# Optimization experiments

Hardware: AMD Instinct MI355X
Metric: run time of the kernel (lower is better)

## Reference

```python
import jax, jax.numpy as jnp
import numpy as np

H = 128          # hidden_size == in_channels == graph_hidden_size
P = 16           # pair_neurons
B = 4096         # number of graph pairs
T = 262144       # total nodes per side
V_D, V_P, V_A = 10000, 4000, 4000          # leaf vocab sizes
NG_D, NG_P, NG_A = 13000, 5200, 5200       # DAG graph node counts
L_D, L_P, L_A = 4, 4, 5                    # ancestor levels
TOTAL_V = V_D + V_P + V_A                  # 18000 rows in all_embedding


def setup_inputs() -> dict:
    key = jax.random.key(0)
    ks = jax.random.split(key, 40)
    n = lambda i, shape, s: jax.random.normal(ks[i], shape, jnp.float32) * s
    ri = lambda i, shape, hi: jax.random.randint(ks[i], shape, 0, hi, dtype=jnp.int64)
    inp = {}
    # forward args
    inp["left_x"] = ri(0, (T, 1), TOTAL_V)
    inp["left_graph_index"] = ri(1, (B,), B)
    inp["right_x"] = ri(2, (T, 1), TOTAL_V)
    inp["right_graph_index"] = ri(3, (B,), B)
    inp["left_x_batch"] = jnp.sort(ri(4, (T,), B))
    inp["right_x_batch"] = jnp.sort(ri(5, (T,), B))
    inp["left_diag_cnt"] = ri(6, (B,), 64)
    inp["right_diag_cnt"] = ri(7, (B,), 64)
    # DAG structure buffers (built by build_ancestors in the original)
    inp["anc_d"] = ri(8, (V_D, L_D), NG_D)
    inp["leaf_d"] = ri(9, (V_D, L_D), NG_D)
    inp["anc_p"] = ri(10, (V_P, L_P), NG_P)
    inp["leaf_p"] = ri(11, (V_P, L_P), NG_P)
    inp["anc_a"] = ri(12, (V_A, L_A), NG_A)
    inp["leaf_a"] = ri(13, (V_A, L_A), NG_A)
    # learned parameters
    inp["emb_d"] = n(14, (NG_D, H), 0.1)
    inp["emb_p"] = n(15, (NG_P, H), 0.1)
    inp["emb_a"] = n(16, (NG_A, H), 0.1)
    inp["Wl_d"] = n(17, (H, 2 * H), 0.05); inp["bl_d"] = n(18, (H,), 0.05); inp["ap_d"] = n(19, (H, 1), 0.05)
    inp["Wl_p"] = n(20, (H, 2 * H), 0.05); inp["bl_p"] = n(21, (H,), 0.05); inp["ap_p"] = n(22, (H, 1), 0.05)
    inp["Wl_a"] = n(23, (H, 2 * H), 0.05); inp["bl_a"] = n(24, (H,), 0.05); inp["ap_a"] = n(25, (H, 1), 0.05)
    inp["W_ntn"] = n(26, (H, H, P), 0.02)
    inp["V_ntn"] = n(27, (P, 2 * H), 0.02)
    inp["b_ntn"] = n(28, (P,), 0.02)
    inp["w_fc"] = n(29, (1, P), 0.1)
    inp["b_fc"] = n(30, (1,), 0.1)
    return inp


def _dag_embedding(emb, anc, leaf, Wl, bl, ap):
    # emb: [Ng,H]; anc/leaf: [V,L] int
    anc_e = emb[anc]    # [V,L,H]
    leaf_e = emb[leaf]  # [V,L,H]
    h = jnp.tanh(jnp.concatenate([anc_e, leaf_e], axis=-1) @ Wl.T + bl)  # [V,L,H]
    aw = (h @ ap)[..., 0]                     # [V,L]
    s = jax.nn.softmax(aw, axis=-1)           # [V,L]
    # torch.matmul((V,L),(V,L,C)).sum(dim=1) == einsum('l,vlc->vc', s.sum(0), anc_e)
    return jnp.einsum('l,vlc->vc', s.sum(axis=0), anc_e)  # [V,H]


def reference(left_x, left_graph_index, right_x, right_graph_index,
              left_x_batch, right_x_batch, left_diag_cnt, right_diag_cnt,
              anc_d, leaf_d, anc_p, leaf_p, anc_a, leaf_a,
              emb_d, emb_p, emb_a,
              Wl_d, bl_d, ap_d, Wl_p, bl_p, ap_p, Wl_a, bl_a, ap_a,
              W_ntn, V_ntn, b_ntn, w_fc, b_fc):
    all_emb = jnp.concatenate([
        _dag_embedding(emb_d, anc_d, leaf_d, Wl_d, bl_d, ap_d),
        _dag_embedding(emb_p, anc_p, leaf_p, Wl_p, bl_p, ap_p),
        _dag_embedding(emb_a, anc_a, leaf_a, Wl_a, bl_a, ap_a),
    ], axis=0)                                  # [TOTAL_V, H]
    left_onto = all_emb[left_x[:, 0]]           # [T,H]
    right_onto = all_emb[right_x[:, 0]]         # [T,H]
    le = jax.ops.segment_sum(left_onto, left_x_batch, num_segments=B)    # [B,H]
    re = jax.ops.segment_sum(right_onto, right_x_batch, num_segments=B)  # [B,H]
    # Neural tensor similarity: tanh(e1^T W_k e2 + V [e1;e2] + b)
    bilinear = jnp.einsum('bi,ijp,bj->bp', le, W_ntn, re)                # [B,P]
    block = jnp.concatenate([le, re], axis=-1) @ V_ntn.T                 # [B,P]
    pair_sim = jnp.tanh(bilinear + block + b_ntn)                        # [B,P]
    out = jax.nn.sigmoid(pair_sim @ w_fc.T + b_fc)[:, 0]                 # [B]
    return out
```

## Files before the change

kernel.cpp:

```cpp
#include <hip/hip_runtime.h>
#include <hip/hip_bf16.h>

typedef __hip_bfloat16 bf16;
typedef __attribute__((ext_vector_type(8))) short bf16x8;
typedef __attribute__((ext_vector_type(4))) float f32x4;

#define HID 128
#define PD  16
#define BB  4096
#define TT  262144
#define VD  10000
#define VP  4000
#define VA  4000
#define NGD 13000
#define NGP 5200
#define NGA 5200

#define NB_D ((NGD + 31) / 32)
#define NB_P ((NGP + 31) / 32)
#define NB_A ((NGA + 31) / 32)

__device__ __forceinline__ float2 bf2x(unsigned int u) {
    float lo = __uint_as_float(u << 16);
    float hi = __uint_as_float(u & 0xffff0000u);
    return make_float2(lo, hi);
}

union Pack2 { bf16 h[2]; unsigned int u; };
__device__ __forceinline__ unsigned int pk2(float a, float b) {
    Pack2 p; p.h[0] = __float2bfloat16(a); p.h[1] = __float2bfloat16(b); return p.u;
}

__global__ __launch_bounds__(256) void prep_b3(
    const float* __restrict__ Wl_d, const float* __restrict__ Wl_p, const float* __restrict__ Wl_a,
    bf16* __restrict__ B3_d, bf16* __restrict__ B3_p, bf16* __restrict__ B3_a)
{
    const int sec = blockIdx.x >> 4, jt = blockIdx.x & 15;
    const float* Wl = (sec == 0) ? Wl_d : (sec == 1) ? Wl_p : Wl_a;
    bf16* B3 = (sec == 0) ? B3_d : (sec == 1) ? B3_p : B3_a;
    const int tid = threadIdx.x;
    const int q = tid >> 6, lane = tid & 63;
    const int quad = lane >> 4, m = lane & 15;
    const int col = jt * 16 + m;
    const float* src = (col < 128) ? (Wl + col * 256) : (Wl + (col - 128) * 256 + 128);
    unsigned int pk[4];
#pragma unroll
    for (int jp = 0; jp < 4; ++jp) {
        int k0 = q * 32 + quad * 8 + 2 * jp;
        pk[jp] = pk2(src[k0], src[k0 + 1]);
    }
    uint4 val = make_uint4(pk[0], pk[1], pk[2], pk[3]);
    *reinterpret_cast<uint4*>(B3 + ((size_t)(jt * 4 + q) * 64 + lane) * 8) = val;
}

__device__ __forceinline__ void stage1_body(
    unsigned short (*Abf)[136],
    const float* __restrict__ emb, const bf16* __restrict__ B3,
    bf16* __restrict__ U, int NG, int blk)
{
    const int tid  = threadIdx.x;
    const int row0 = blk * 32;
    {
        const int r = tid >> 3, seg = tid & 7;
        const int g = row0 + r;
        float v[16];
        if (g < NG) {
            const float4* src = reinterpret_cast<const float4*>(emb + (size_t)g * HID + seg * 16);
#pragma unroll
            for (int i = 0; i < 4; ++i) {
                float4 f = src[i];
                v[4 * i] = f.x; v[4 * i + 1] = f.y; v[4 * i + 2] = f.z; v[4 * i + 3] = f.w;
            }
        } else {
#pragma unroll
            for (int i = 0; i < 16; ++i) v[i] = 0.f;
        }
        unsigned int pk[8];
#pragma unroll
        for (int i = 0; i < 8; ++i) pk[i] = pk2(v[2 * i], v[2 * i + 1]);
        uint4* dst = reinterpret_cast<uint4*>(&Abf[r][seg * 16]);
        dst[0] = make_uint4(pk[0], pk[1], pk[2], pk[3]);
        dst[1] = make_uint4(pk[4], pk[5], pk[6], pk[7]);
    }
    __syncthreads();

    const int lane   = tid & 63;
    const int w      = tid >> 6;
    const int gtile  = w & 1;
    const int jstrip = w >> 1;
    const int lrow   = gtile * 16 + (lane & 15);
    const int koff   = (lane >> 4) * 8;
    const bf16x8* B3f = reinterpret_cast<const bf16x8*>(B3);

    f32x4 acc[8];
#pragma unroll
    for (int t = 0; t < 8; ++t) acc[t] = (f32x4){0.f, 0.f, 0.f, 0.f};

#pragma unroll
    for (int q = 0; q < 4; ++q) {
        bf16x8 ef = *reinterpret_cast<const bf16x8*>(&Abf[lrow][q * 32 + koff]);
#pragma unroll
        for (int t = 0; t < 8; ++t) {
            int jt = jstrip * 8 + t;
            bf16x8 wf = B3f[(jt * 4 + q) * 64 + lane];
            acc[t] = __builtin_amdgcn_mfma_f32_16x16x32_bf16(wf, ef, acc[t], 0, 0, 0);
        }
    }

    const int g = row0 + gtile * 16 + (lane & 15);
    if (g < NG) {
        const int quad = lane >> 4;
        bf16* Ur = U + (size_t)g * 256;
#pragma unroll
        for (int t = 0; t < 8; ++t) {
            int j0 = (jstrip * 8 + t) * 16 + quad * 4;
            uint2 st = make_uint2(pk2(acc[t].x, acc[t].y), pk2(acc[t].z, acc[t].w));
            *reinterpret_cast<uint2*>(Ur + j0) = st;
        }
    }
}

__global__ __launch_bounds__(256) void stage1_mfma(
    const float* __restrict__ emb_d, const bf16* __restrict__ B3_d, bf16* __restrict__ U_d,
    const float* __restrict__ emb_p, const bf16* __restrict__ B3_p, bf16* __restrict__ U_p,
    const float* __restrict__ emb_a, const bf16* __restrict__ B3_a, bf16* __restrict__ U_a)
{
    __shared__ unsigned short Abf[32][136];
    int bx = blockIdx.x;
    if (bx < NB_D)             stage1_body(Abf, emb_d, B3_d, U_d, NGD, bx);
    else if (bx < NB_D + NB_P) stage1_body(Abf, emb_p, B3_p, U_p, NGP, bx - NB_D);
    else                       stage1_body(Abf, emb_a, B3_a, U_a, NGA, bx - NB_D - NB_P);
}

template <int L>
__device__ __forceinline__ void aw_body(
    float* sacc,
    const bf16* __restrict__ U, const int* __restrict__ anc, const int* __restrict__ leaf,
    const float* __restrict__ bl, const float* __restrict__ ap,
    float* __restrict__ s_out, int V, int blk, int nblk)
{
    const int tid  = threadIdx.x;
    const int lane = tid & 63;
    const int wid  = blk * 4 + (tid >> 6);
    const int nw   = nblk * 4;
    const float2 blv = *reinterpret_cast<const float2*>(bl + 2 * lane);
    const float2 apv = *reinterpret_cast<const float2*>(ap + 2 * lane);
    const unsigned int* Uw = reinterpret_cast<const unsigned int*>(U);
    float wacc[L];
#pragma unroll
    for (int l = 0; l < L; ++l) wacc[l] = 0.f;

    for (int vp = wid; vp < V / 2; vp += nw) {
        const int v0 = 2 * vp;
        int a0[L], f0[L], a1[L], f1[L];
        if (L == 4) {
            int4 ia = *reinterpret_cast<const int4*>(anc  + (size_t)v0 * 4);
            int4 ib = *reinterpret_cast<const int4*>(anc  + (size_t)v0 * 4 + 4);
            int4 fa = *reinterpret_cast<const int4*>(leaf + (size_t)v0 * 4);
            int4 fb = *reinterpret_cast<const int4*>(leaf + (size_t)v0 * 4 + 4);
            a0[0] = ia.x; a0[1] = ia.y; a0[2] = ia.z; a0[3] = ia.w;
            a1[0] = ib.x; a1[1] = ib.y; a1[2] = ib.z; a1[3] = ib.w;
            f0[0] = fa.x; f0[1] = fa.y; f0[2] = fa.z; f0[3] = fa.w;
            f1[0] = fb.x; f1[1] = fb.y; f1[2] = fb.z; f1[3] = fb.w;
        } else {
#pragma unroll
            for (int l = 0; l < L; ++l) {
                a0[l] = anc[(size_t)v0 * L + l];
                a1[l] = anc[(size_t)(v0 + 1) * L + l];
                f0[l] = leaf[(size_t)v0 * L + l];
                f1[l] = leaf[(size_t)(v0 + 1) * L + l];
            }
        }
        unsigned int ua0[L], ul0[L], ua1[L], ul1[L];
#pragma unroll
        for (int l = 0; l < L; ++l) {
            ua0[l] = Uw[(size_t)a0[l] * 128 + lane];
            ul0[l] = Uw[(size_t)f0[l] * 128 + 64 + lane];
            ua1[l] = Uw[(size_t)a1[l] * 128 + lane];
            ul1[l] = Uw[(size_t)f1[l] * 128 + 64 + lane];
        }
        float aw0[L], aw1[L];
#pragma unroll
        for (int l = 0; l < L; ++l) {
            float2 x0 = bf2x(ua0[l]), y0 = bf2x(ul0[l]);
            float2 x1 = bf2x(ua1[l]), y1 = bf2x(ul1[l]);
            float p0 = tanhf(x0.x + y0.x + blv.x) * apv.x + tanhf(x0.y + y0.y + blv.y) * apv.y;
            float p1 = tanhf(x1.x + y1.x + blv.x) * apv.x + tanhf(x1.y + y1.y + blv.y) * apv.y;
#pragma unroll
            for (int off = 32; off; off >>= 1) {
                p0 += __shfl_xor(p0, off, 64);
                p1 += __shfl_xor(p1, off, 64);
            }
            aw0[l] = p0; aw1[l] = p1;
        }
        float m0 = aw0[0], m1 = aw1[0];
#pragma unroll
        for (int l = 1; l < L; ++l) { m0 = fmaxf(m0, aw0[l]); m1 = fmaxf(m1, aw1[l]); }
        float d0 = 0.f, d1 = 0.f, e0[L], e1[L];
#pragma unroll
        for (int l = 0; l < L; ++l) {
            e0[l] = __expf(aw0[l] - m0); d0 += e0[l];
            e1[l] = __expf(aw1[l] - m1); d1 += e1[l];
        }
        float i0 = 1.f / d0, i1 = 1.f / d1;
#pragma unroll
        for (int l = 0; l < L; ++l) wacc[l] += e0[l] * i0 + e1[l] * i1;
    }
    if (lane == 0) {
#pragma unroll
        for (int l = 0; l < L; ++l) atomicAdd(&sacc[l], wacc[l]);
    }
    __syncthreads();
    if (tid < L) atomicAdd(&s_out[tid], sacc[tid]);
}

__global__ __launch_bounds__(256) void aw_all(
    const bf16* __restrict__ U_d, const int* __restrict__ anc_d, const int* __restrict__ leaf_d,
    const float* __restrict__ bl_d, const float* __restrict__ ap_d,
    const bf16* __restrict__ U_p, const int* __restrict__ anc_p, const int* __restrict__ leaf_p,
    const float* __restrict__ bl_p, const float* __restrict__ ap_p,
    const bf16* __restrict__ U_a, const int* __restrict__ anc_a, const int* __restrict__ leaf_a,
    const float* __restrict__ bl_a, const float* __restrict__ ap_a,
    float* __restrict__ s_sum)
{
    __shared__ float sacc[5];
    const int tid = threadIdx.x;
    if (tid < 5) sacc[tid] = 0.f;
    __syncthreads();
    int bx = blockIdx.x;
    if (bx < 512)      aw_body<4>(sacc, U_d, anc_d, leaf_d, bl_d, ap_d, s_sum + 0, VD, bx, 512);
    else if (bx < 768) aw_body<4>(sacc, U_p, anc_p, leaf_p, bl_p, ap_p, s_sum + 4, VP, bx - 512, 256);
    else               aw_body<5>(sacc, U_a, anc_a, leaf_a, bl_a, ap_a, s_sum + 8, VA, bx - 768, 256);
}

template <int L>
__device__ __forceinline__ void allemb_body(
    const float* __restrict__ emb, const int* __restrict__ anc,
    const float* __restrict__ s, float* __restrict__ out, int V, int blk, int nblk)
{
    const int tid   = threadIdx.x;
    const int lane4 = tid & 31;
    const int vslot = tid >> 5;
    const float4* emb4 = reinterpret_cast<const float4*>(emb);
    float4* out4 = reinterpret_cast<float4*>(out);
    float sv[L];
#pragma unroll
    for (int l = 0; l < L; ++l) sv[l] = s[l];
    for (int vp = blk * 8 + vslot; vp < V / 2; vp += nblk * 8) {
        const int v0 = 2 * vp;
        int a0[L], a1[L];
        if (L == 4) {
            int4 ia = *reinterpret_cast<const int4*>(anc + (size_t)v0 * 4);
            int4 ib = *reinterpret_cast<const int4*>(anc + (size_t)v0 * 4 + 4);
            a0[0] = ia.x; a0[1] = ia.y; a0[2] = ia.z; a0[3] = ia.w;
            a1[0] = ib.x; a1[1] = ib.y; a1[2] = ib.z; a1[3] = ib.w;
        } else {
#pragma unroll
            for (int l = 0; l < L; ++l) {
                a0[l] = anc[(size_t)v0 * L + l];
                a1[l] = anc[(size_t)(v0 + 1) * L + l];
            }
        }
        float4 e0[L], e1[L];
#pragma unroll
        for (int l = 0; l < L; ++l) {
            e0[l] = emb4[(size_t)a0[l] * 32 + lane4];
            e1[l] = emb4[(size_t)a1[l] * 32 + lane4];
        }
        float4 r0 = make_float4(0.f, 0.f, 0.f, 0.f);
        float4 r1 = make_float4(0.f, 0.f, 0.f, 0.f);
#pragma unroll
        for (int l = 0; l < L; ++l) {
            r0.x += sv[l] * e0[l].x; r0.y += sv[l] * e0[l].y;
            r0.z += sv[l] * e0[l].z; r0.w += sv[l] * e0[l].w;
            r1.x += sv[l] * e1[l].x; r1.y += sv[l] * e1[l].y;
            r1.z += sv[l] * e1[l].z; r1.w += sv[l] * e1[l].w;
        }
        out4[(size_t)v0 * 32 + lane4]       = r0;
        out4[(size_t)(v0 + 1) * 32 + lane4] = r1;
    }
}

__global__ __launch_bounds__(256) void allemb_all(
    const float* __restrict__ emb_d, const int* __restrict__ anc_d,
    const float* __restrict__ emb_p, const int* __restrict__ anc_p,
    const float* __restrict__ emb_a, const int* __restrict__ anc_a,
    const float* __restrict__ s_sum, float* __restrict__ all_emb)
{
    int bx = blockIdx.x;
    if (bx < 512)
        allemb_body<4>(emb_d, anc_d, s_sum + 0, all_emb, VD, bx, 512);
    else if (bx < 768)
        allemb_body<4>(emb_p, anc_p, s_sum + 4, all_emb + (size_t)VD * HID, VP, bx - 512, 256);
    else
        allemb_body<5>(emb_a, anc_a, s_sum + 8, all_emb + (size_t)(VD + VP) * HID, VA, bx - 768, 256);
}

__global__ __launch_bounds__(256) void seg_bounds(
    const int* __restrict__ lb, const int* __restrict__ rb,
    int* __restrict__ segL, int* __restrict__ segR, float* __restrict__ s_sum)
{
    int gid = blockIdx.x * 256 + threadIdx.x;
    if (gid >= 2 * BB + 8 && gid < 2 * BB + 24) s_sum[gid - (2 * BB + 8)] = 0.f;
    const int* batch;
    int* segp;
    int b;
    if (gid <= BB) { batch = lb; segp = segL; b = gid; }
    else if (gid <= 2 * BB + 1) { batch = rb; segp = segR; b = gid - BB - 1; }
    else return;
    int l = 0, r = TT;
    while (l < r) { int m = (l + r) >> 1; if (batch[m] < b) l = m + 1; else r = m; }
    segp[b] = l;
}

__global__ __launch_bounds__(256) void segsum_mlp(
    const float* __restrict__ all_emb,
    const int* __restrict__ lx, const int* __restrict__ segL, float* __restrict__ le,
    const int* __restrict__ rx, const int* __restrict__ segR, float* __restrict__ re)
{
    __shared__ float4 red[4][32];
    const int tid  = threadIdx.x;
    const int b    = blockIdx.x & (BB - 1);
    const int lane = tid & 63;
    const int w    = tid >> 6;
    const int* x;
    const int* seg;
    float* out;
    if (blockIdx.x < BB) { x = lx; seg = segL; out = le; }
    else                 { x = rx; seg = segR; out = re; }
    const int lo = seg[b], hi = seg[b + 1];
    const int half  = lane >> 5;
    const int lane4 = lane & 31;
    const float4* AE4 = reinterpret_cast<const float4*>(all_emb);
    float4 acc = make_float4(0.f, 0.f, 0.f, 0.f);

    for (int tb = lo + 16 * w; tb < hi; tb += 64) {
        int idxv = x[min(tb + (lane & 15), hi - 1)];
        float4 v[8];
        int val[8];
#pragma unroll
        for (int u = 0; u < 8; ++u) {
            int src = 2 * u + half;
            int ridx = __shfl(idxv, src, 64);
            val[u] = (tb + src) < hi;
            v[u] = AE4[(size_t)ridx * 32 + lane4];
        }
#pragma unroll
        for (int u = 0; u < 8; ++u) {
            if (val[u]) {
                acc.x += v[u].x; acc.y += v[u].y;
                acc.z += v[u].z; acc.w += v[u].w;
            }
        }
    }
    acc.x += __shfl_xor(acc.x, 32, 64);
    acc.y += __shfl_xor(acc.y, 32, 64);
    acc.z += __shfl_xor(acc.z, 32, 64);
    acc.w += __shfl_xor(acc.w, 32, 64);
    if (lane < 32) red[w][lane4] = acc;
    __syncthreads();
    if (tid < 32) {
        float4 r0 = red[0][tid], r1 = red[1][tid], r2 = red[2][tid], r3 = red[3][tid];
        float4 s;
        s.x = r0.x + r1.x + r2.x + r3.x;
        s.y = r0.y + r1.y + r2.y + r3.y;
        s.z = r0.z + r1.z + r2.z + r3.z;
        s.w = r0.w + r1.w + r2.w + r3.w;
        reinterpret_cast<float4*>(out)[(size_t)b * 32 + tid] = s;
    }
}

__global__ __launch_bounds__(256) void ntn_part(
    const float* __restrict__ le, const float* __restrict__ re,
    const float* __restrict__ W2, float* __restrict__ part)
{
    __shared__ float Alds[32][68];
    __shared__ float Blds[32 * 264];
    __shared__ float Rlds[64][17];
    const int tid   = threadIdx.x;
    const int row0  = blockIdx.x * 64;
    const int col0  = blockIdx.y * 256;
    const int lane5 = tid & 31;
    const int rbase = (tid >> 5) * 8;
    const int cbase = lane5 * 8;
    float acc[8][8];
#pragma unroll
    for (int i = 0; i < 8; ++i)
#pragma unroll
        for (int j = 0; j < 8; ++j) acc[i][j] = 0.f;

    for (int i = tid; i < 64 * 16; i += 256) {
        int rr = i >> 4, jl = i & 15;
        Rlds[rr][jl] = re[(size_t)(row0 + rr) * HID + blockIdx.y * 16 + jl];
    }

    for (int k0 = 0; k0 < 128; k0 += 32) {
        __syncthreads();
        for (int i = tid; i < 64 * 32; i += 256) {
            int rr = i >> 5, kk = i & 31;
            Alds[kk][rr] = le[(size_t)(row0 + rr) * HID + k0 + kk];
        }
        for (int i = tid; i < 32 * 64; i += 256) {
            int kk = i >> 6, j4 = (i & 63) * 4;
            float4 v = *reinterpret_cast<const float4*>(&W2[(size_t)(k0 + kk) * 2048 + col0 + j4]);
            *reinterpret_cast<float4*>(&Blds[kk * 264 + j4]) = v;
        }
        __syncthreads();
#pragma unroll
        for (int kk = 0; kk < 32; ++kk) {
            float4 a0 = *reinterpret_cast<const float4*>(&Alds[kk][rbase]);
            float4 a1 = *reinterpret_cast<const float4*>(&Alds[kk][rbase + 4]);
            float4 b0 = *reinterpret_cast<const float4*>(&Blds[kk * 264 + cbase]);
            float4 b1 = *reinterpret_cast<const float4*>(&Blds[kk * 264 + cbase + 4]);
            float av[8] = {a0.x, a0.y, a0.z, a0.w, a1.x, a1.y, a1.z, a1.w};
            float bv[8] = {b0.x, b0.y, b0.z, b0.w, b1.x, b1.y, b1.z, b1.w};
#pragma unroll
            for (int i = 0; i < 8; ++i)
#pragma unroll
                for (int j = 0; j < 8; ++j) acc[i][j] += av[i] * bv[j];
        }
    }

    const int jloc = lane5 >> 1;
    const int pq   = (tid & 1) * 8;
#pragma unroll
    for (int i = 0; i < 8; ++i) {
        int row = rbase + i;
        float rj = Rlds[row][jloc];
        float pb[8];
#pragma unroll
        for (int j = 0; j < 8; ++j) pb[j] = acc[i][j] * rj;
#pragma unroll
        for (int m = 2; m <= 16; m <<= 1) {
#pragma unroll
            for (int j = 0; j < 8; ++j) pb[j] += __shfl_xor(pb[j], m, 64);
        }
        if ((tid & 30) == 0) {
            size_t base = ((size_t)blockIdx.y * BB + row0 + row) * PD + pq;
            *reinterpret_cast<float4*>(&part[base])     = make_float4(pb[0], pb[1], pb[2], pb[3]);
            *reinterpret_cast<float4*>(&part[base + 4]) = make_float4(pb[4], pb[5], pb[6], pb[7]);
        }
    }
}

__global__ __launch_bounds__(256) void ntn_epi(
    const float* __restrict__ part, const float* __restrict__ le, const float* __restrict__ re,
    const float* __restrict__ Vntn, const float* __restrict__ bntn,
    const float* __restrict__ wfc, const float* __restrict__ bfc,
    float* __restrict__ out)
{
    __shared__ float Vlds[16 * 257];
    __shared__ float LE[16 * 128];
    __shared__ float RE[16 * 128];
    const int tid = threadIdx.x;
    const int b0  = blockIdx.x * 16;
    for (int i = tid; i < 4096; i += 256) Vlds[(i >> 8) * 257 + (i & 255)] = Vntn[i];
    for (int i = tid; i < 2048; i += 256) {
        LE[i] = le[(size_t)b0 * HID + i];
        RE[i] = re[(size_t)b0 * HID + i];
    }
    __syncthreads();
    const int bl = tid >> 4, p = tid & 15;
    const int b  = b0 + bl;
    float bil = 0.f;
#pragma unroll
    for (int by = 0; by < 8; ++by) bil += part[((size_t)by * BB + b) * PD + p];
    float s = bil + bntn[p];
    const float* Vp   = &Vlds[p * 257];
    const float* lrow = &LE[bl * 128];
    const float* rrow = &RE[bl * 128];
#pragma unroll 8
    for (int c = 0; c < 128; ++c) s += lrow[c] * Vp[c] + rrow[c] * Vp[128 + c];
    float x = tanhf(s) * wfc[p];
    x += __shfl_xor(x, 1, 64);
    x += __shfl_xor(x, 2, 64);
    x += __shfl_xor(x, 4, 64);
    x += __shfl_xor(x, 8, 64);
    if (p == 0) out[b] = 1.f / (1.f + __expf(-(x + bfc[0])));
}

extern "C" void kernel_launch(void* const* d_in, const int* in_sizes, int n_in,
                              void* d_out, int out_size, void* d_ws, size_t ws_size,
                              hipStream_t stream)
{
    const int* left_x      = (const int*)d_in[0];
    const int* right_x     = (const int*)d_in[2];
    const int* left_batch  = (const int*)d_in[4];
    const int* right_batch = (const int*)d_in[5];
    const int* anc_d  = (const int*)d_in[8];
    const int* leaf_d = (const int*)d_in[9];
    const int* anc_p  = (const int*)d_in[10];
    const int* leaf_p = (const int*)d_in[11];
    const int* anc_a  = (const int*)d_in[12];
    const int* leaf_a = (const int*)d_in[13];
    const float* emb_d = (const float*)d_in[14];
    const float* emb_p = (const float*)d_in[15];
    const float* emb_a = (const float*)d_in[16];
    const float* Wl_d = (const float*)d_in[17];
    const float* bl_d = (const float*)d_in[18];
    const float* ap_d = (const float*)d_in[19];
    const float* Wl_p = (const float*)d_in[20];
    const float* bl_p = (const float*)d_in[21];
    const float* ap_p = (const float*)d_in[22];
    const float* Wl_a = (const float*)d_in[23];
    const float* bl_a = (const float*)d_in[24];
    const float* ap_a = (const float*)d_in[25];
    const float* W_ntn = (const float*)d_in[26];
    const float* V_ntn = (const float*)d_in[27];
    const float* b_ntn = (const float*)d_in[28];
    const float* w_fc  = (const float*)d_in[29];
    const float* b_fc  = (const float*)d_in[30];
    float* out = (float*)d_out;

    float* ws = (float*)d_ws;
    float* s_sum   = ws;
    float* le      = ws + 64;
    float* re      = le + (size_t)BB * HID;
    float* all_emb = re + (size_t)BB * HID;
    float* part    = all_emb + (size_t)(VD + VP + VA) * HID;
    int*   segL    = (int*)(part + (size_t)8 * BB * PD);
    int*   segR    = segL + 4100;
    bf16*  U       = (bf16*)(segR + 4100);
    bf16*  U_d = U;
    bf16*  U_p = U_d + (size_t)NGD * 256;
    bf16*  U_a = U_p + (size_t)NGP * 256;
    bf16*  B3_d = U_a + (size_t)NGA * 256;
    bf16*  B3_p = B3_d + 32768;
    bf16*  B3_a = B3_p + 32768;

    prep_b3<<<48, 256, 0, stream>>>(Wl_d, Wl_p, Wl_a, B3_d, B3_p, B3_a);

    seg_bounds<<<33, 256, 0, stream>>>(left_batch, right_batch, segL, segR, s_sum);

    stage1_mfma<<<NB_D + NB_P + NB_A, 256, 0, stream>>>(
        emb_d, B3_d, U_d, emb_p, B3_p, U_p, emb_a, B3_a, U_a);

    aw_all<<<1024, 256, 0, stream>>>(
        U_d, anc_d, leaf_d, bl_d, ap_d,
        U_p, anc_p, leaf_p, bl_p, ap_p,
        U_a, anc_a, leaf_a, bl_a, ap_a, s_sum);

    allemb_all<<<1024, 256, 0, stream>>>(
        emb_d, anc_d, emb_p, anc_p, emb_a, anc_a, s_sum, all_emb);

    segsum_mlp<<<2 * BB, 256, 0, stream>>>(
        all_emb, left_x, segL, le, right_x, segR, re);

    ntn_part<<<dim3(64, 8), 256, 0, stream>>>(le, re, W_ntn, part);

    ntn_epi<<<BB / 16, 256, 0, stream>>>(part, le, re, V_ntn, b_ntn, w_fc, b_fc, out);
}
```

Before: 235.1 us.

## Retile NTN bilinear kernel to 32-row blocks with interleaved column mapping

Shrinks the ntn_part tile from 64 to 32 rows per block, doubling the grid to 1024 blocks, and cuts per-thread accumulators from 8x8 to 4x8. Each lane now reads two contiguous float4 slices of B that are 128 columns apart, and A is stored row-major with padding. The j-reduction is rewritten to combine the low and high halves before the shuffle tree. The aim is more occupancy and more blocks across the CUs, at the cost of less register reuse per loaded element and a smaller arithmetic intensity per tile.

```diff
diff --git a/kernel.cpp b/kernel.cpp
--- a/kernel.cpp
+++ b/kernel.cpp
@@ -370,75 +370,80 @@
     }
 }
 
-__global__ __launch_bounds__(256) void ntn_part(
+__global__ __launch_bounds__(256, 4) void ntn_part(
     const float* __restrict__ le, const float* __restrict__ re,
     const float* __restrict__ W2, float* __restrict__ part)
 {
-    __shared__ float Alds[32][68];
-    __shared__ float Blds[32 * 264];
-    __shared__ float Rlds[64][17];
+    __shared__ float Alds[32][33];
+    __shared__ float Blds[32 * 256];
+    __shared__ float Rlds[32][17];
     const int tid   = threadIdx.x;
-    const int row0  = blockIdx.x * 64;
-    const int col0  = blockIdx.y * 256;
+    const int row0  = blockIdx.x * 32;
+    const int ch    = blockIdx.y;
+    const int col0  = ch * 256;
     const int lane5 = tid & 31;
-    const int rbase = (tid >> 5) * 8;
-    const int cbase = lane5 * 8;
-    float acc[8][8];
-#pragma unroll
-    for (int i = 0; i < 8; ++i)
+    const int h     = tid >> 5;
+    const int rbase = h * 4;
+    float acc[4][8];
+#pragma unroll
+    for (int i = 0; i < 4; ++i)
 #pragma unroll
         for (int j = 0; j < 8; ++j) acc[i][j] = 0.f;
 
-    for (int i = tid; i < 64 * 16; i += 256) {
+    for (int i = tid; i < 32 * 16; i += 256) {
         int rr = i >> 4, jl = i & 15;
-        Rlds[rr][jl] = re[(size_t)(row0 + rr) * HID + blockIdx.y * 16 + jl];
+        Rlds[rr][jl] = re[(size_t)(row0 + rr) * HID + ch * 16 + jl];
     }
 
     for (int k0 = 0; k0 < 128; k0 += 32) {
         __syncthreads();
-        for (int i = tid; i < 64 * 32; i += 256) {
-            int rr = i >> 5, kk = i & 31;
-            Alds[kk][rr] = le[(size_t)(row0 + rr) * HID + k0 + kk];
+        {
+            const int rr = tid >> 5, kk = tid & 31;
+#pragma unroll
+            for (int it = 0; it < 4; ++it)
+                Alds[rr + it * 8][kk] = le[(size_t)(row0 + rr + it * 8) * HID + k0 + kk];
         }
         for (int i = tid; i < 32 * 64; i += 256) {
             int kk = i >> 6, j4 = (i & 63) * 4;
             float4 v = *reinterpret_cast<const float4*>(&W2[(size_t)(k0 + kk) * 2048 + col0 + j4]);
-            *reinterpret_cast<float4*>(&Blds[kk * 264 + j4]) = v;
+            *reinterpret_cast<float4*>(&Blds[kk * 256 + j4]) = v;
         }
         __syncthreads();
 #pragma unroll
         for (int kk = 0; kk < 32; ++kk) {
-            float4 a0 = *reinterpret_cast<const float4*>(&Alds[kk][rbase]);
-            float4 a1 = *reinterpret_cast<const float4*>(&Alds[kk][rbase + 4]);
-            float4 b0 = *reinterpret_cast<const float4*>(&Blds[kk * 264 + cbase]);
-            float4 b1 = *reinterpret_cast<const float4*>(&Blds[kk * 264 + cbase + 4]);
-            float av[8] = {a0.x, a0.y, a0.z, a0.w, a1.x, a1.y, a1.z, a1.w};
-            float bv[8] = {b0.x, b0.y, b0.z, b0.w, b1.x, b1.y, b1.z, b1.w};
-#pragma unroll
-            for (int i = 0; i < 8; ++i)
-#pragma unroll
-                for (int j = 0; j < 8; ++j) acc[i][j] += av[i] * bv[j];
-        }
-    }
-
-    const int jloc = lane5 >> 1;
-    const int pq   = (tid & 1) * 8;
-#pragma unroll
-    for (int i = 0; i < 8; ++i) {
-        int row = rbase + i;
-        float rj = Rlds[row][jloc];
-        float pb[8];
-#pragma unroll
-        for (int j = 0; j < 8; ++j) pb[j] = acc[i][j] * rj;
-#pragma unroll
-        for (int m = 2; m <= 16; m <<= 1) {
-#pragma unroll
-            for (int j = 0; j < 8; ++j) pb[j] += __shfl_xor(pb[j], m, 64);
-        }
-        if ((tid & 30) == 0) {
-            size_t base = ((size_t)blockIdx.y * BB + row0 + row) * PD + pq;
-            *reinterpret_cast<float4*>(&part[base])     = make_float4(pb[0], pb[1], pb[2], pb[3]);
-            *reinterpret_cast<float4*>(&part[base + 4]) = make_float4(pb[4], pb[5], pb[6], pb[7]);
+            float4 blo = *reinterpret_cast<const float4*>(&Blds[kk * 256 + 4 * lane5]);
+            float4 bhi = *reinterpret_cast<const float4*>(&Blds[kk * 256 + 128 + 4 * lane5]);
+            float a0 = Alds[rbase + 0][kk];
+            float a1 = Alds[rbase + 1][kk];
+            float a2 = Alds[rbase + 2][kk];
+            float a3 = Alds[rbase + 3][kk];
+            acc[0][0] += a0 * blo.x; acc[0][1] += a0 * blo.y; acc[0][2] += a0 * blo.z; acc[0][3] += a0 * blo.w;
+            acc[0][4] += a0 * bhi.x; acc[0][5] += a0 * bhi.y; acc[0][6] += a0 * bhi.z; acc[0][7] += a0 * bhi.w;
+            acc[1][0] += a1 * blo.x; acc[1][1] += a1 * blo.y; acc[1][2] += a1 * blo.z; acc[1][3] += a1 * blo.w;
+            acc[1][4] += a1 * bhi.x; acc[1][5] += a1 * bhi.y; acc[1][6] += a1 * bhi.z; acc[1][7] += a1 * bhi.w;
+            acc[2][0] += a2 * blo.x; acc[2][1] += a2 * blo.y; acc[2][2] += a2 * blo.z; acc[2][3] += a2 * blo.w;
+            acc[2][4] += a2 * bhi.x; acc[2][5] += a2 * bhi.y; acc[2][6] += a2 * bhi.z; acc[2][7] += a2 * bhi.w;
+            acc[3][0] += a3 * blo.x; acc[3][1] += a3 * blo.y; acc[3][2] += a3 * blo.z; acc[3][3] += a3 * blo.w;
+            acc[3][4] += a3 * bhi.x; acc[3][5] += a3 * bhi.y; acc[3][6] += a3 * bhi.z; acc[3][7] += a3 * bhi.w;
+        }
+    }
+
+    const int q = lane5 >> 2;
+#pragma unroll
+    for (int r = 0; r < 4; ++r) {
+        float rlo = Rlds[rbase + r][q];
+        float rhi = Rlds[rbase + r][8 + q];
+        float pb[4];
+#pragma unroll
+        for (int d = 0; d < 4; ++d) pb[d] = acc[r][d] * rlo + acc[r][4 + d] * rhi;
+#pragma unroll
+        for (int m = 4; m <= 16; m <<= 1) {
+#pragma unroll
+            for (int d = 0; d < 4; ++d) pb[d] += __shfl_xor(pb[d], m, 64);
+        }
+        if (lane5 < 4) {
+            size_t base = ((size_t)ch * BB + row0 + rbase + r) * PD + 4 * lane5;
+            *reinterpret_cast<float4*>(&part[base]) = make_float4(pb[0], pb[1], pb[2], pb[3]);
         }
     }
 }
@@ -546,7 +551,7 @@
     segsum_mlp<<<2 * BB, 256, 0, stream>>>(
         all_emb, left_x, segL, le, right_x, segR, re);
 
-    ntn_part<<<dim3(64, 8), 256, 0, stream>>>(le, re, W_ntn, part);
+    ntn_part<<<dim3(128, 8), 256, 0, stream>>>(le, re, W_ntn, part);
 
     ntn_epi<<<BB / 16, 256, 0, stream>>>(part, le, re, V_ntn, b_ntn, w_fc, b_fc, out);
 }
```

Measured after the change: 295.4 us. 1.26x slower.
